# Kernel optimization log

Measured on AMD Instinct MI355X. Metric: run time of the kernel, lower is better.

The kernel has to match this reference:

```python
import jax, jax.numpy as jnp
import numpy as np


def conv2d(x, w, b=None, pad=0):
    out = jax.lax.conv_general_dilated(
        x, w, window_strides=(1, 1), padding=[(pad, pad), (pad, pad)],
        dimension_numbers=('NCHW', 'OIHW', 'NCHW'))
    if b is not None:
        out = out + b[None, :, None, None]
    return out


def maxpool2(x):
    return jax.lax.reduce_window(x, -jnp.inf, jax.lax.max,
                                 (1, 1, 2, 2), (1, 1, 2, 2), 'VALID')


def conv_offset_2d(x, offset_w):
    """ConvOffset2D: learn per-pixel (dy,dx) offsets via a 3x3 conv (C->2C, no
    bias), then bilinearly resample x at grid+offset. Faithful to the repo,
    including its raw (B,2C,H,W)->(B*C,H,W,2) memory reinterpretation."""
    B, C, H, W = x.shape
    off = conv2d(x, offset_w, pad=1)                  # (B, 2C, H, W)
    off = off.reshape(B * C, H, W, 2)                 # raw row-major reshape (as in repo)
    xf = x.reshape(B * C, H, W)
    gy, gx = jnp.meshgrid(jnp.arange(H, dtype=x.dtype),
                          jnp.arange(W, dtype=x.dtype), indexing='ij')
    coords = off + jnp.stack([gy, gx], axis=-1)       # (BC, H, W, 2) = (y, x)
    cy = jnp.clip(coords[..., 0], 0.0, float(H - 1))
    cx = jnp.clip(coords[..., 1], 0.0, float(W - 1))
    y0 = jnp.floor(cy)
    x0 = jnp.floor(cx)
    y0i = y0.astype(jnp.int32)
    x0i = x0.astype(jnp.int32)
    y1i = jnp.ceil(cy).astype(jnp.int32)
    x1i = jnp.ceil(cx).astype(jnp.int32)
    bidx = jnp.arange(B * C)[:, None, None]
    v_lt = xf[bidx, y0i, x0i]
    v_rt = xf[bidx, y0i, x1i]
    v_lb = xf[bidx, y1i, x0i]
    v_rb = xf[bidx, y1i, x1i]
    tx = cx - x0
    ty = cy - y0
    v_t = v_lt + (v_rt - v_lt) * tx
    v_b = v_lb + (v_rb - v_lb) * tx
    out = v_t + (v_b - v_t) * ty
    return out.reshape(B, C, H, W)


def setup_inputs() -> dict:
    key = jax.random.key(0)
    ks = jax.random.split(key, 9)
    B = 2048
    inp = {
        'x': jax.random.normal(ks[0], (B, 1, 28, 28), dtype=jnp.float32),
        'off1_w': jax.random.normal(ks[1], (2, 1, 3, 3), dtype=jnp.float32) * 0.01,
        'conv1_w': jax.random.normal(ks[2], (16, 1, 5, 5), dtype=jnp.float32) * 0.1,
        'conv1_b': jax.random.normal(ks[3], (16,), dtype=jnp.float32) * 0.01,
        'off2_w': jax.random.normal(ks[4], (32, 16, 3, 3), dtype=jnp.float32) * 0.01,
        'conv2_w': jax.random.normal(ks[5], (32, 16, 5, 5), dtype=jnp.float32) * 0.05,
        'conv2_b': jax.random.normal(ks[6], (32,), dtype=jnp.float32) * 0.01,
        'fc_w': jax.random.normal(ks[7], (10, 32 * 7 * 7), dtype=jnp.float32) * 0.02,
        'fc_b': jax.random.normal(ks[8], (10,), dtype=jnp.float32) * 0.01,
    }
    return inp


def reference(x, off1_w, conv1_w, conv1_b, off2_w, conv2_w, conv2_b, fc_w, fc_b):
    # block 1: deform sample -> 5x5 conv pad 2 -> relu -> maxpool 2
    h = conv_offset_2d(x, off1_w)
    h = maxpool2(jax.nn.relu(conv2d(h, conv1_w, conv1_b, pad=2)))   # (B,16,14,14)
    # block 2
    h = conv_offset_2d(h, off2_w)
    h = maxpool2(jax.nn.relu(conv2d(h, conv2_w, conv2_b, pad=2)))   # (B,32,7,7)
    # classifier
    flat = h.reshape(h.shape[0], -1)                                # (B, 1568)
    return flat @ fc_w.T + fc_b
```

## Files before the change

kernel.cpp:

```cpp
#include <hip/hip_runtime.h>
#include <hip/hip_bf16.h>


#define B_IMG 2048

typedef short bf16x8 __attribute__((ext_vector_type(8)));
typedef float f32x4 __attribute__((ext_vector_type(4)));

__global__ __launch_bounds__(256) void k_prep(const float* __restrict__ w_off2,
                                              const float* __restrict__ w_c2,
                                              __hip_bfloat16* __restrict__ wqo,
                                              __hip_bfloat16* __restrict__ wq2) {
    int e = blockIdx.x * 256 + threadIdx.x;
    if (e < 5120) {
        int sp = e >> 10, rem = e & 1023, oc = rem >> 5, k = rem & 31;
        int sl = k >> 4, ic = k & 15, s = 2 * sp + sl;
        wqo[e] = __float2bfloat16(s < 9 ? w_off2[(oc * 16 + ic) * 9 + s] : 0.f);
    } else if (e < 18432) {
        int e2 = e - 5120;
        int sp = e2 >> 10, rem = e2 & 1023, oc = rem >> 5, k = rem & 31;
        int sl = k >> 4, ic = k & 15, s = 2 * sp + sl;
        wq2[e2] = __float2bfloat16(s < 25 ? w_c2[(oc * 16 + ic) * 25 + s] : 0.f);
    }
}

__global__ __launch_bounds__(256, 5) void k_net(const float* __restrict__ x,
                                                const float* __restrict__ off1_w,
                                                const float* __restrict__ conv1_w,
                                                const float* __restrict__ conv1_b,
                                                const __hip_bfloat16* __restrict__ wqo,
                                                const __hip_bfloat16* __restrict__ wq2,
                                                const float* __restrict__ conv2_b,
                                                const float* __restrict__ fc_w,
                                                const float* __restrict__ fc_b,
                                                float* __restrict__ out) {
    __shared__ __align__(16) char s5[12544];
    __shared__ __align__(16) __hip_bfloat16 imgb[17 * 16 * 16];
    __shared__ __align__(16) __hip_bfloat16 img2b[18 * 20 * 16];

    float* xs    = (float*)s5;
    float* img2  = (float*)(s5 + 3600);
    float* wsc   = (float*)(s5 + 7696);
    float* bsc   = (float*)(s5 + 9296);
    _Float16* offbuf = (_Float16*)s5;
    float* pl    = (float*)s5;
    float* wredp = (float*)(s5 + 6272);

    int b = blockIdx.x, t = threadIdx.x;

    for (int i = t; i < 900; i += 256) xs[i] = 0.f;
    for (int i = t; i < 1024; i += 256) img2[i] = 0.f;
    for (int i = t; i < 2176; i += 256) ((unsigned int*)imgb)[i] = 0u;
    for (int i = t; i < 2880; i += 256) ((unsigned int*)img2b)[i] = 0u;
    for (int i = t; i < 400; i += 256) wsc[i] = conv1_w[i];
    if (t < 16) bsc[t] = conv1_b[t];
    __syncthreads();
    for (int i = t; i < 784; i += 256)
        xs[(i / 28 + 1) * 30 + (i % 28) + 1] = x[b * 784 + i];
    __syncthreads();

    for (int p = t; p < 784; p += 256) {
        int h = p / 28, w = p % 28;
        float off[2];
        int flat0 = h * 56 + w * 2;
#pragma unroll
        for (int k = 0; k < 2; ++k) {
            int flat = flat0 + k;
            int c = flat / 784;
            int r = flat % 784;
            int hh = r / 28, ww = r % 28;
            float s = 0.f;
#pragma unroll
            for (int dy = 0; dy < 3; ++dy)
#pragma unroll
                for (int dx = 0; dx < 3; ++dx)
                    s += off1_w[c * 9 + dy * 3 + dx] * xs[(hh + dy) * 30 + ww + dx];
            off[k] = s;
        }
        float cy = fminf(fmaxf((float)h + off[0], 0.f), 27.f);
        float cx = fminf(fmaxf((float)w + off[1], 0.f), 27.f);
        float y0f = floorf(cy), x0f = floorf(cx);
        int y0 = (int)y0f, x0 = (int)x0f;
        int y1 = (int)ceilf(cy), x1 = (int)ceilf(cx);
        float ty = cy - y0f, tx = cx - x0f;
        float vlt = xs[(y0 + 1) * 30 + x0 + 1], vrt = xs[(y0 + 1) * 30 + x1 + 1];
        float vlb = xs[(y1 + 1) * 30 + x0 + 1], vrb = xs[(y1 + 1) * 30 + x1 + 1];
        float vt = vlt + (vrt - vlt) * tx;
        float vb = vlb + (vrb - vlb) * tx;
        img2[(h + 2) * 32 + (w + 2)] = vt + (vb - vt) * ty;
    }
    __syncthreads();

    {
        int oc = t & 15;
        float wv[25];
#pragma unroll
        for (int q = 0; q < 25; ++q) wv[q] = wsc[oc * 25 + q];
        float bv = bsc[oc];
        for (int o = t; o < 1568; o += 256) {
            int r = o >> 4;
            int i = r / 7, jp = r % 7;
            float s_[2][4];
#pragma unroll
            for (int py = 0; py < 2; ++py)
#pragma unroll
                for (int cx = 0; cx < 4; ++cx) s_[py][cx] = bv;
#pragma unroll
            for (int q = 0; q < 6; ++q) {
                const float4* rp = (const float4*)&img2[(2 * i + q) * 32 + 4 * jp];
                float4 ra = rp[0], rb = rp[1];
                float row[8] = {ra.x, ra.y, ra.z, ra.w, rb.x, rb.y, rb.z, rb.w};
#pragma unroll
                for (int py = 0; py < 2; ++py) {
                    int dy = q - py;
                    if (dy >= 0 && dy < 5) {
#pragma unroll
                        for (int cx = 0; cx < 4; ++cx)
#pragma unroll
                            for (int dx = 0; dx < 5; ++dx)
                                s_[py][cx] += wv[dy * 5 + dx] * row[cx + dx];
                    }
                }
            }
            float m0 = fmaxf(fmaxf(s_[0][0], s_[0][1]), fmaxf(s_[1][0], s_[1][1]));
            float m1 = fmaxf(fmaxf(s_[0][2], s_[0][3]), fmaxf(s_[1][2], s_[1][3]));
            m0 = fmaxf(m0, 0.f);
            m1 = fmaxf(m1, 0.f);
            imgb[(i + 1) * 256 + (2 * jp + 1) * 16 + oc] = __float2bfloat16(m0);
            imgb[(i + 1) * 256 + (2 * jp + 2) * 16 + oc] = __float2bfloat16(m1);
        }
    }
    __syncthreads();

    int wv_ = t >> 6, li = t & 63;
    int och = wv_ & 1, yh = wv_ >> 1;
    int nrows = yh ? 6 : 8;
    int lx = li & 15, lg = li >> 4;

    {
        const bf16x8* wA = (const bf16x8*)wqo;
        bf16x8 afA[5];
#pragma unroll
        for (int sp = 0; sp < 5; ++sp)
            afA[sp] = wA[(sp * 32 + och * 16 + lx) * 4 + lg];
        int slA = lg >> 1, icsel = lg & 1;
        f32x4 acc[8];
#pragma unroll
        for (int y = 0; y < 8; ++y) acc[y] = (f32x4){0.f, 0.f, 0.f, 0.f};
        const bf16x8* ib = (const bf16x8*)imgb;
#pragma unroll
        for (int sp = 0; sp < 5; ++sp) {
            int s0 = 2 * sp + slA;
            int dy = s0 / 3, dx = s0 % 3;
            if (s0 >= 9) { dy = 0; dx = 0; }
            int base = dy * 32 + (lx + dx) * 2 + icsel;
#pragma unroll
            for (int y = 0; y < 8; ++y) {
                if (y < nrows) {
                    bf16x8 bfr = ib[base + (yh * 8 + y) * 32];
                    acc[y] = __builtin_amdgcn_mfma_f32_16x16x32_bf16(afA[sp], bfr, acc[y], 0, 0, 0);
                }
            }
        }
        if (lx < 14) {
#pragma unroll
            for (int y = 0; y < 8; ++y) {
                if (y < nrows) {
                    int yy = yh * 8 + y;
#pragma unroll
                    for (int r = 0; r < 4; ++r) {
                        int oc = och * 16 + lg * 4 + r;
                        offbuf[oc * 196 + yy * 14 + lx] = (_Float16)acc[y][r];
                    }
                }
            }
        }
    }
    __syncthreads();

    for (int o = t; o < 3136; o += 256) {
        int c = o & 15, rem = o >> 4;
        int h = rem / 14, w = rem % 14;
        int flat0 = c * 392 + h * 28 + w * 2;
        float offy = (float)offbuf[flat0];
        float offx = (float)offbuf[flat0 + 1];
        float cy = fminf(fmaxf((float)h + offy, 0.f), 13.f);
        float cx = fminf(fmaxf((float)w + offx, 0.f), 13.f);
        float y0f = floorf(cy), x0f = floorf(cx);
        int y0 = (int)y0f, x0 = (int)x0f;
        int y1 = (int)ceilf(cy), x1 = (int)ceilf(cx);
        float ty = cy - y0f, tx = cx - x0f;
        float vlt = __bfloat162float(imgb[(y0 + 1) * 256 + (x0 + 1) * 16 + c]);
        float vrt = __bfloat162float(imgb[(y0 + 1) * 256 + (x1 + 1) * 16 + c]);
        float vlb = __bfloat162float(imgb[(y1 + 1) * 256 + (x0 + 1) * 16 + c]);
        float vrb = __bfloat162float(imgb[(y1 + 1) * 256 + (x1 + 1) * 16 + c]);
        float vt = vlt + (vrt - vlt) * tx;
        float vb = vlb + (vrb - vlb) * tx;
        img2b[((h + 2) * 20 + (w + 2)) * 16 + c] = __float2bfloat16(vt + (vb - vt) * ty);
    }
    __syncthreads();

    {
        const bf16x8* wB = (const bf16x8*)wq2;
        bf16x8 af[13];
#pragma unroll
        for (int sp = 0; sp < 13; ++sp)
            af[sp] = wB[(sp * 32 + och * 16 + lx) * 4 + lg];
        int sl = lg >> 1, icg = lg & 1;
        float bias_r[4];
#pragma unroll
        for (int r = 0; r < 4; ++r) bias_r[r] = conv2_b[och * 16 + lg * 4 + r];
        f32x4 acc[8];
#pragma unroll
        for (int y = 0; y < 8; ++y) acc[y] = (f32x4){0.f, 0.f, 0.f, 0.f};
        const bf16x8* ib2 = (const bf16x8*)img2b;
#pragma unroll
        for (int sp = 0; sp < 13; ++sp) {
            int s0 = 2 * sp + sl;
            int dy = s0 / 5, dx = s0 % 5;
            if (s0 >= 25) { dy = 0; dx = 0; }
            int base = (lx + dx) * 2 + icg;
#pragma unroll
            for (int y = 0; y < 8; ++y) {
                if (y < nrows) {
                    bf16x8 bfr = ib2[base + (yh * 8 + y + dy) * 40];
                    acc[y] = __builtin_amdgcn_mfma_f32_16x16x32_bf16(af[sp], bfr, acc[y], 0, 0, 0);
                }
            }
        }
        __syncthreads();
        int npool = yh ? 3 : 4;
#pragma unroll
        for (int u = 0; u < 4; ++u) {
            if (u < npool) {
                int i = yh * 4 + u;
#pragma unroll
                for (int r = 0; r < 4; ++r) {
                    int oc = och * 16 + lg * 4 + r;
                    float v = fmaxf(fmaxf(acc[2 * u][r], acc[2 * u + 1][r]) + bias_r[r], 0.f);
                    float p = __shfl_xor(v, 1);
                    float m = fmaxf(v, p);
                    if (((lx & 1) == 0) && lx < 14)
                        pl[oc * 49 + i * 7 + (lx >> 1)] = m;
                }
            }
        }
    }
    __syncthreads();

    float facc[10];
#pragma unroll
    for (int o = 0; o < 10; ++o) facc[o] = 0.f;
#pragma unroll
    for (int it = 0; it < 2; ++it) {
        int k = t * 4 + it * 1024;
        if (k < 1568) {
            float4 v = *(const float4*)&pl[k];
#pragma unroll
            for (int o = 0; o < 10; ++o) {
                float4 w4 = *(const float4*)&fc_w[o * 1568 + k];
                facc[o] += v.x * w4.x + v.y * w4.y + v.z * w4.z + v.w * w4.w;
            }
        }
    }
#pragma unroll
    for (int o = 0; o < 10; ++o) {
        float s = facc[o];
#pragma unroll
        for (int m = 32; m > 0; m >>= 1) s += __shfl_xor(s, m);
        if (li == 0) wredp[o * 4 + wv_] = s;
    }
    __syncthreads();
    if (t < 10)
        out[b * 10 + t] = fc_b[t] + wredp[t * 4] + wredp[t * 4 + 1] + wredp[t * 4 + 2] + wredp[t * 4 + 3];
}

extern "C" void kernel_launch(void* const* d_in, const int* in_sizes, int n_in,
                              void* d_out, int out_size, void* d_ws, size_t ws_size,
                              hipStream_t stream) {
    const float* x       = (const float*)d_in[0];
    const float* off1_w  = (const float*)d_in[1];
    const float* conv1_w = (const float*)d_in[2];
    const float* conv1_b = (const float*)d_in[3];
    const float* off2_w  = (const float*)d_in[4];
    const float* conv2_w = (const float*)d_in[5];
    const float* conv2_b = (const float*)d_in[6];
    const float* fc_w    = (const float*)d_in[7];
    const float* fc_b    = (const float*)d_in[8];
    float* out = (float*)d_out;

    char* ws = (char*)d_ws;
    __hip_bfloat16* wqo = (__hip_bfloat16*)ws;
    __hip_bfloat16* wq2 = (__hip_bfloat16*)(ws + 10240);

    k_prep<<<72, 256, 0, stream>>>(off2_w, conv2_w, wqo, wq2);
    k_net<<<B_IMG, 256, 0, stream>>>(x, off1_w, conv1_w, conv1_b, wqo, wq2,
                                     conv2_b, fc_w, fc_b, out);
}
```

Before: 70.08 us.

## Compute conv1 with bf16 MFMA im2col and fused ReLU-maxpool via shuffles

Moves the first 5x5 convolution from scalar FP32 FMAs to 16x16x32 bf16 MFMA instructions. The sampled image is stored in bf16 in shared memory, and each lane gathers a 25-tap im2col fragment against conv1 weights pre-packed by the prep kernel. Bias, ReLU and 2x2 maxpool are fused into the MFMA epilogue using a lane shuffle. This drops conv1 to bf16 precision, adds scattered per-element LDS gathers, and lowers the occupancy hint from 5 to 4 blocks.

```diff
diff --git a/kernel.cpp b/kernel.cpp
--- a/kernel.cpp
+++ b/kernel.cpp
@@ -9,8 +9,10 @@
 
 __global__ __launch_bounds__(256) void k_prep(const float* __restrict__ w_off2,
                                               const float* __restrict__ w_c2,
+                                              const float* __restrict__ w_c1,
                                               __hip_bfloat16* __restrict__ wqo,
-                                              __hip_bfloat16* __restrict__ wq2) {
+                                              __hip_bfloat16* __restrict__ wq2,
+                                              __hip_bfloat16* __restrict__ wqc1) {
     int e = blockIdx.x * 256 + threadIdx.x;
     if (e < 5120) {
         int sp = e >> 10, rem = e & 1023, oc = rem >> 5, k = rem & 31;
@@ -21,12 +23,16 @@
         int sp = e2 >> 10, rem = e2 & 1023, oc = rem >> 5, k = rem & 31;
         int sl = k >> 4, ic = k & 15, s = 2 * sp + sl;
         wq2[e2] = __float2bfloat16(s < 25 ? w_c2[(oc * 16 + ic) * 25 + s] : 0.f);
+    } else if (e < 18944) {
+        int e3 = e - 18432;
+        int oc = e3 >> 5, k = e3 & 31;
+        wqc1[e3] = __float2bfloat16(k < 25 ? w_c1[oc * 25 + k] : 0.f);
     }
 }
 
-__global__ __launch_bounds__(256, 5) void k_net(const float* __restrict__ x,
+__global__ __launch_bounds__(256, 4) void k_net(const float* __restrict__ x,
                                                 const float* __restrict__ off1_w,
-                                                const float* __restrict__ conv1_w,
+                                                const __hip_bfloat16* __restrict__ wqc1,
                                                 const float* __restrict__ conv1_b,
                                                 const __hip_bfloat16* __restrict__ wqo,
                                                 const __hip_bfloat16* __restrict__ wq2,
@@ -38,10 +44,8 @@
     __shared__ __align__(16) __hip_bfloat16 imgb[17 * 16 * 16];
     __shared__ __align__(16) __hip_bfloat16 img2b[18 * 20 * 16];
 
-    float* xs    = (float*)s5;
-    float* img2  = (float*)(s5 + 3600);
-    float* wsc   = (float*)(s5 + 7696);
-    float* bsc   = (float*)(s5 + 9296);
+    float* xs = (float*)s5;
+    __hip_bfloat16* img2bf = (__hip_bfloat16*)(s5 + 3600);
     _Float16* offbuf = (_Float16*)s5;
     float* pl    = (float*)s5;
     float* wredp = (float*)(s5 + 6272);
@@ -49,11 +53,9 @@
     int b = blockIdx.x, t = threadIdx.x;
 
     for (int i = t; i < 900; i += 256) xs[i] = 0.f;
-    for (int i = t; i < 1024; i += 256) img2[i] = 0.f;
+    for (int i = t; i < 576; i += 256) ((unsigned int*)img2bf)[i] = 0u;
     for (int i = t; i < 2176; i += 256) ((unsigned int*)imgb)[i] = 0u;
     for (int i = t; i < 2880; i += 256) ((unsigned int*)img2b)[i] = 0u;
-    for (int i = t; i < 400; i += 256) wsc[i] = conv1_w[i];
-    if (t < 16) bsc[t] = conv1_b[t];
     __syncthreads();
     for (int i = t; i < 784; i += 256)
         xs[(i / 28 + 1) * 30 + (i % 28) + 1] = x[b * 784 + i];
@@ -87,55 +89,68 @@
         float vlb = xs[(y1 + 1) * 30 + x0 + 1], vrb = xs[(y1 + 1) * 30 + x1 + 1];
         float vt = vlt + (vrt - vlt) * tx;
         float vb = vlb + (vrb - vlb) * tx;
-        img2[(h + 2) * 32 + (w + 2)] = vt + (vb - vt) * ty;
-    }
-    __syncthreads();
+        img2bf[(h + 2) * 36 + (w + 2)] = __float2bfloat16(vt + (vb - vt) * ty);
+    }
+    __syncthreads();
+
+    int wv_ = t >> 6, li = t & 63;
+    int lx = li & 15, lg = li >> 4;
 
     {
-        int oc = t & 15;
-        float wv[25];
-#pragma unroll
-        for (int q = 0; q < 25; ++q) wv[q] = wsc[oc * 25 + q];
-        float bv = bsc[oc];
-        for (int o = t; o < 1568; o += 256) {
-            int r = o >> 4;
-            int i = r / 7, jp = r % 7;
-            float s_[2][4];
-#pragma unroll
-            for (int py = 0; py < 2; ++py)
-#pragma unroll
-                for (int cx = 0; cx < 4; ++cx) s_[py][cx] = bv;
-#pragma unroll
-            for (int q = 0; q < 6; ++q) {
-                const float4* rp = (const float4*)&img2[(2 * i + q) * 32 + 4 * jp];
-                float4 ra = rp[0], rb = rp[1];
-                float row[8] = {ra.x, ra.y, ra.z, ra.w, rb.x, rb.y, rb.z, rb.w};
-#pragma unroll
-                for (int py = 0; py < 2; ++py) {
-                    int dy = q - py;
-                    if (dy >= 0 && dy < 5) {
-#pragma unroll
-                        for (int cx = 0; cx < 4; ++cx)
-#pragma unroll
-                            for (int dx = 0; dx < 5; ++dx)
-                                s_[py][cx] += wv[dy * 5 + dx] * row[cx + dx];
+        const bf16x8* wc1v = (const bf16x8*)wqc1;
+        bf16x8 af1 = wc1v[lx * 4 + lg];
+        float b4[4];
+#pragma unroll
+        for (int r = 0; r < 4; ++r) b4[r] = conv1_b[lg * 4 + r];
+        int ypstart = (wv_ < 2) ? wv_ * 4 : 8 + (wv_ - 2) * 3;
+        int ypcnt = (wv_ < 2) ? 4 : 3;
+        const unsigned short* ib28 = (const unsigned short*)img2bf;
+        for (int u = 0; u < 4; ++u) {
+            if (u < ypcnt) {
+                int yp = ypstart + u;
+#pragma unroll
+                for (int xh = 0; xh < 2; ++xh) {
+                    int xp = xh * 16 + lx;
+                    f32x4 a0 = (f32x4){0.f, 0.f, 0.f, 0.f};
+                    f32x4 a1 = (f32x4){0.f, 0.f, 0.f, 0.f};
+#pragma unroll
+                    for (int yy = 0; yy < 2; ++yy) {
+                        int y = 2 * yp + yy;
+                        unsigned short uu[8];
+#pragma unroll
+                        for (int j = 0; j < 8; ++j) {
+                            int tt = 8 * lg + j;
+                            int dyq = tt / 5;
+                            int dxq = tt - 5 * dyq;
+                            unsigned short v = 0;
+                            if (tt < 25) v = ib28[(y + dyq) * 36 + xp + dxq];
+                            uu[j] = v;
+                        }
+                        bf16x8 bq = {(short)uu[0], (short)uu[1], (short)uu[2], (short)uu[3],
+                                     (short)uu[4], (short)uu[5], (short)uu[6], (short)uu[7]};
+                        if (yy == 0)
+                            a0 = __builtin_amdgcn_mfma_f32_16x16x32_bf16(af1, bq, a0, 0, 0, 0);
+                        else
+                            a1 = __builtin_amdgcn_mfma_f32_16x16x32_bf16(af1, bq, a1, 0, 0, 0);
                     }
-                }
-            }
-            float m0 = fmaxf(fmaxf(s_[0][0], s_[0][1]), fmaxf(s_[1][0], s_[1][1]));
-            float m1 = fmaxf(fmaxf(s_[0][2], s_[0][3]), fmaxf(s_[1][2], s_[1][3]));
-            m0 = fmaxf(m0, 0.f);
-            m1 = fmaxf(m1, 0.f);
-            imgb[(i + 1) * 256 + (2 * jp + 1) * 16 + oc] = __float2bfloat16(m0);
-            imgb[(i + 1) * 256 + (2 * jp + 2) * 16 + oc] = __float2bfloat16(m1);
-        }
-    }
-    __syncthreads();
-
-    int wv_ = t >> 6, li = t & 63;
+#pragma unroll
+                    for (int r = 0; r < 4; ++r) {
+                        float v = fmaxf(fmaxf(a0[r], a1[r]) + b4[r], 0.f);
+                        float p = __shfl_xor(v, 1);
+                        float m = fmaxf(v, p);
+                        if (((xp & 1) == 0) && xp < 28) {
+                            int oc = lg * 4 + r;
+                            imgb[(yp + 1) * 256 + ((xp >> 1) + 1) * 16 + oc] = __float2bfloat16(m);
+                        }
+                    }
+                }
+            }
+        }
+    }
+    __syncthreads();
+
     int och = wv_ & 1, yh = wv_ >> 1;
     int nrows = yh ? 6 : 8;
-    int lx = li & 15, lg = li >> 4;
 
     {
         const bf16x8* wA = (const bf16x8*)wqo;
@@ -290,10 +305,11 @@
     float* out = (float*)d_out;
 
     char* ws = (char*)d_ws;
-    __hip_bfloat16* wqo = (__hip_bfloat16*)ws;
-    __hip_bfloat16* wq2 = (__hip_bfloat16*)(ws + 10240);
-
-    k_prep<<<72, 256, 0, stream>>>(off2_w, conv2_w, wqo, wq2);
-    k_net<<<B_IMG, 256, 0, stream>>>(x, off1_w, conv1_w, conv1_b, wqo, wq2,
+    __hip_bfloat16* wqo  = (__hip_bfloat16*)ws;
+    __hip_bfloat16* wq2  = (__hip_bfloat16*)(ws + 10240);
+    __hip_bfloat16* wqc1 = (__hip_bfloat16*)(ws + 36864);
+
+    k_prep<<<74, 256, 0, stream>>>(off2_w, conv2_w, conv1_w, wqo, wq2, wqc1);
+    k_net<<<B_IMG, 256, 0, stream>>>(x, off1_w, wqc1, conv1_b, wqo, wq2,
                                      conv2_b, fc_w, fc_b, out);
 }
```

New measurement: 61.26 us. 12.6% less time.
